# Kernel tuning notes

Hardware: AMD Instinct MI355X
Metric: run time of the kernel (lower is better)

Reference implementation:

```python
import math
import jax, jax.numpy as jnp
import numpy as np

B, S, HID = 1, 2048, 4096
NH, NKV, D = 32, 8, 128
THETA = 10000.0


def setup_inputs() -> dict:
    key = jax.random.key(0)
    k1, k2, k3, k4, k5 = jax.random.split(key, 5)
    hidden_states = jax.random.normal(k1, (B, S, HID), dtype=jnp.float32)
    k_cache = jax.random.normal(k2, (B, NKV, S, D), dtype=jnp.float32)
    v_cache = jax.random.normal(k3, (B, NKV, S, D), dtype=jnp.float32)
    Wq = jax.random.normal(k4, (HID, NH * D), dtype=jnp.float32) * 0.02
    Wo = jax.random.normal(k5, (NH * D, HID), dtype=jnp.float32) * 0.02
    position_ids = jnp.broadcast_to(jnp.arange(S, dtype=jnp.int32), (B, S))
    # causal mask: True = masked out (torch.where(mask, -10000, scores))
    attention_mask = jnp.broadcast_to(
        jnp.triu(jnp.ones((S, S), dtype=bool), k=1)[None, None], (B, 1, S, S)
    )
    return {
        "hidden_states": hidden_states,
        "k_cache": k_cache,
        "v_cache": v_cache,
        "Wq": Wq,
        "Wo": Wo,
        "position_ids": position_ids,
        "attention_mask": attention_mask,
    }


def _rotate_half(x):
    x1, x2 = jnp.split(x, 2, axis=-1)
    return jnp.concatenate([-x2, x1], axis=-1)


def _rope_tables(position_ids):
    # Llama rotary embedding gathered at position_ids -> [B, 1, S, D]
    inv_freq = 1.0 / (THETA ** (jnp.arange(0, D, 2, dtype=jnp.float32) / D))
    freqs = position_ids[..., None].astype(jnp.float32) * inv_freq  # [B, S, D/2]
    emb = jnp.concatenate([freqs, freqs], axis=-1)  # [B, S, D]
    return jnp.cos(emb)[:, None], jnp.sin(emb)[:, None]


def reference(hidden_states, k_cache, v_cache, Wq, Wo, position_ids, attention_mask):
    G = NH // NKV  # GQA group size
    # q projection: [B, S, HID] -> [B, NH, S, D]
    q = (hidden_states @ Wq).reshape(B, S, NH, D).transpose(0, 2, 1, 3)
    cos, sin = _rope_tables(position_ids)
    q = q * cos + _rotate_half(q) * sin
    # GQA without materializing repeat_kv: group query heads over kv heads
    qg = q.reshape(B, NKV, G, S, D)
    scores = jnp.einsum("bkgsd,bktd->bkgst", qg, k_cache) / math.sqrt(D)
    scores = scores.reshape(B, NH, S, S)
    scores = jnp.where(attention_mask, jnp.float32(-10000.0), scores)
    probs = jax.nn.softmax(scores.astype(jnp.float32), axis=-1).astype(q.dtype)
    out = jnp.einsum("bkgst,bktd->bkgsd", probs.reshape(B, NKV, G, S, S), v_cache)
    out = out.reshape(B, NH, S, D).transpose(0, 2, 1, 3).reshape(B, S, NH * D)
    return out @ Wo
```

## Files before the change

### kernel.cpp

```cpp
#include <hip/hip_runtime.h>
#include <cstdint>
#include <cstddef>

#define S_LEN 2048
#define HID 4096
#define NH 32
#define NKV 8
#define HD 128

typedef __attribute__((ext_vector_type(4))) float f32x4;
typedef __attribute__((ext_vector_type(8))) short bf16x8;

__device__ __forceinline__ unsigned short f2bf(float f) {
  union { float f; uint32_t u; } v; v.f = f;
  uint32_t r = v.u + 0x7FFFu + ((v.u >> 16) & 1u);
  return (unsigned short)(r >> 16);
}

__device__ __forceinline__ float exp2_fast(float x) {
#if __has_builtin(__builtin_amdgcn_exp2f)
  return __builtin_amdgcn_exp2f(x);
#else
  float r; asm("v_exp_f32 %0, %1" : "=v"(r) : "v"(x)); return r;
#endif
}

__device__ __forceinline__ unsigned int cvt_pk_bf16(float lo, float hi) {
  unsigned int r;
  asm("v_cvt_pk_bf16_f32 %0, %1, %2" : "=v"(r) : "v"(lo), "v"(hi));
  return r;
}

__global__ void cvt_bf16_kernel(const float* __restrict__ in,
                                unsigned short* __restrict__ out, int n4) {
  int i = blockIdx.x * blockDim.x + threadIdx.x;
  if (i >= n4) return;
  float4 v = ((const float4*)in)[i];
  ushort4 o;
  o.x = f2bf(v.x); o.y = f2bf(v.y); o.z = f2bf(v.z); o.w = f2bf(v.w);
  ((ushort4*)out)[i] = o;
}

__global__ __launch_bounds__(256) void transpose_cvt2_kernel(
    const float* __restrict__ in0, unsigned short* __restrict__ out0,
    const float* __restrict__ in1, unsigned short* __restrict__ out1,
    int R, int C) {
  __shared__ float tile[64][65];
  const float* inb = (blockIdx.z == 0) ? in0 : in1;
  unsigned short* outb = (blockIdx.z == 0) ? out0 : out1;
  const int c0 = blockIdx.x * 64, r0 = blockIdx.y * 64;
  const int tid = threadIdx.x;
#pragma unroll
  for (int p = 0; p < 4; ++p) {
    const int ch = p * 256 + tid;
    const int r = ch >> 4, off = (ch & 15) << 2;
    *(float4*)&tile[r][off] = *(const float4*)(inb + (size_t)(r0 + r) * C + c0 + off);
  }
  __syncthreads();
#pragma unroll
  for (int p = 0; p < 2; ++p) {
    const int ch = p * 256 + tid;
    const int i = ch >> 3, j0 = (ch & 7) << 3;
    bf16x8 v;
#pragma unroll
    for (int k = 0; k < 8; ++k) v[k] = (short)f2bf(tile[j0 + k][i]);
    *(bf16x8*)(outb + (size_t)(c0 + i) * R + r0 + j0) = v;
  }
}

__global__ __launch_bounds__(256) void transpose_cvt_kernel(
    const float* __restrict__ in, unsigned short* __restrict__ out, int R, int C) {
  __shared__ float tile[64][65];
  const int b = blockIdx.z;
  const float* inb = in + (size_t)b * R * C;
  unsigned short* outb = out + (size_t)b * R * C;
  const int c0 = blockIdx.x * 64, r0 = blockIdx.y * 64;
  const int tid = threadIdx.x;
#pragma unroll
  for (int p = 0; p < 4; ++p) {
    const int ch = p * 256 + tid;
    const int r = ch >> 4, off = (ch & 15) << 2;
    *(float4*)&tile[r][off] = *(const float4*)(inb + (size_t)(r0 + r) * C + c0 + off);
  }
  __syncthreads();
#pragma unroll
  for (int p = 0; p < 2; ++p) {
    const int ch = p * 256 + tid;
    const int i = ch >> 3, j0 = (ch & 7) << 3;
    bf16x8 v;
#pragma unroll
    for (int k = 0; k < 8; ++k) v[k] = (short)f2bf(tile[j0 + k][i]);
    *(bf16x8*)(outb + (size_t)(c0 + i) * R + r0 + j0) = v;
  }
}

__global__ __launch_bounds__(256, 2) void gemm_bt_kernel(
    const unsigned short* __restrict__ A, const unsigned short* __restrict__ BT,
    float* __restrict__ C, int M, int N, int K) {
  __shared__ __align__(16) unsigned short As[128 * 64];
  __shared__ __align__(16) unsigned short Bs[128 * 64];
  const int tid = threadIdx.x;
  const int lane = tid & 63;
  const int wid = tid >> 6;
  const int wm = (wid >> 1) * 64, wn = (wid & 1) * 64;
  const int g = blockIdx.x;
  const int xcd = g & 7, local = g >> 3;
  const int m0 = (xcd * 2 + (local & 1)) * 128;
  const int n0 = (local >> 1) * 128;
  const int lr = lane & 15;
  const int quad = lane >> 4;
  const int sw = lr & 7;
  f32x4 acc[4][4] = {};
  for (int kt = 0; kt < K; kt += 64) {
    __syncthreads();
#pragma unroll
    for (int p = 0; p < 4; ++p) {
      const int c = p * 256 + tid;
      const int r = c >> 3, jsrc = (c & 7) ^ (r & 7);
      __builtin_amdgcn_global_load_lds(
          (const __attribute__((address_space(1))) void*)(A + (size_t)(m0 + r) * K + kt + jsrc * 8),
          (__attribute__((address_space(3))) void*)(As + c * 8), 16, 0, 0);
      __builtin_amdgcn_global_load_lds(
          (const __attribute__((address_space(1))) void*)(BT + (size_t)(n0 + r) * K + kt + jsrc * 8),
          (__attribute__((address_space(3))) void*)(Bs + c * 8), 16, 0, 0);
    }
    __syncthreads();
#pragma unroll
    for (int h = 0; h < 2; ++h) {
      const int pos = ((h * 4 + quad) ^ sw) << 3;
      bf16x8 a[4], b[4];
#pragma unroll
      for (int t = 0; t < 4; ++t) {
        a[t] = *(const bf16x8*)(As + (wm + t * 16 + lr) * 64 + pos);
        b[t] = *(const bf16x8*)(Bs + (wn + t * 16 + lr) * 64 + pos);
      }
#pragma unroll
      for (int mt = 0; mt < 4; ++mt)
#pragma unroll
        for (int nt = 0; nt < 4; ++nt)
          acc[mt][nt] = __builtin_amdgcn_mfma_f32_16x16x32_bf16(a[mt], b[nt], acc[mt][nt], 0, 0, 0);
    }
  }
  const int qd = quad << 2;
#pragma unroll
  for (int mt = 0; mt < 4; ++mt)
#pragma unroll
    for (int nt = 0; nt < 4; ++nt) {
      const int row = m0 + wm + mt * 16 + qd;
      const int col = n0 + wn + nt * 16 + lr;
#pragma unroll
      for (int r = 0; r < 4; ++r)
        C[(size_t)(row + r) * N + col] = acc[mt][nt][r];
    }
}

__global__ __launch_bounds__(256, 2) void gemm_rope_kernel(
    const unsigned short* __restrict__ A, const unsigned short* __restrict__ BT,
    const int* __restrict__ pos_ids, unsigned short* __restrict__ Qout) {
  __shared__ __align__(16) unsigned short As[128 * 64];
  __shared__ __align__(16) unsigned short Bs[128 * 64];
  const int tid = threadIdx.x;
  const int lane = tid & 63;
  const int wid = tid >> 6;
  const int wm = wid * 32;
  const int g = blockIdx.x;
  const int xcd = g & 7, local = g >> 3;
  const int m0 = (xcd * 2 + (local & 1)) * 128;
  const int n0 = (local >> 1) * 128;
  const int lr = lane & 15;
  const int quad = lane >> 4;
  const int sw = lr & 7;
  f32x4 acc[2][8] = {};
  for (int kt = 0; kt < HID; kt += 64) {
    __syncthreads();
#pragma unroll
    for (int p = 0; p < 4; ++p) {
      const int c = p * 256 + tid;
      const int r = c >> 3, jsrc = (c & 7) ^ (r & 7);
      __builtin_amdgcn_global_load_lds(
          (const __attribute__((address_space(1))) void*)(A + (size_t)(m0 + r) * HID + kt + jsrc * 8),
          (__attribute__((address_space(3))) void*)(As + c * 8), 16, 0, 0);
      __builtin_amdgcn_global_load_lds(
          (const __attribute__((address_space(1))) void*)(BT + (size_t)(n0 + r) * HID + kt + jsrc * 8),
          (__attribute__((address_space(3))) void*)(Bs + c * 8), 16, 0, 0);
    }
    __syncthreads();
#pragma unroll
    for (int h = 0; h < 2; ++h) {
      const int pos = ((h * 4 + quad) ^ sw) << 3;
      bf16x8 a[2], b[8];
#pragma unroll
      for (int t = 0; t < 2; ++t)
        a[t] = *(const bf16x8*)(As + (wm + t * 16 + lr) * 64 + pos);
#pragma unroll
      for (int t = 0; t < 8; ++t)
        b[t] = *(const bf16x8*)(Bs + (t * 16 + lr) * 64 + pos);
#pragma unroll
      for (int mt = 0; mt < 2; ++mt)
#pragma unroll
        for (int nt = 0; nt < 8; ++nt)
          acc[mt][nt] = __builtin_amdgcn_mfma_f32_16x16x32_bf16(a[mt], b[nt], acc[mt][nt], 0, 0, 0);
    }
  }
  const int qd = quad << 2;
  const int h = n0 >> 7;
#pragma unroll
  for (int mt = 0; mt < 2; ++mt)
#pragma unroll
    for (int r = 0; r < 4; ++r) {
      const int row = m0 + wm + mt * 16 + qd + r;
      const float pos = (float)pos_ids[row];
#pragma unroll
      for (int nt = 0; nt < 4; ++nt) {
        const int i = nt * 16 + lr;
        const float invf = __expf(-(float)(2 * i) * (9.2103403719761836f / 128.0f));
        float sn, cs;
        __sincosf(pos * invf, &sn, &cs);
        const float x1 = acc[mt][nt][r], x2 = acc[mt][nt + 4][r];
        Qout[((size_t)h * S_LEN + row) * HD + i]      = f2bf(x1 * cs - x2 * sn);
        Qout[((size_t)h * S_LEN + row) * HD + i + 64] = f2bf(x2 * cs + x1 * sn);
      }
    }
}

__global__ __launch_bounds__(256, 2) void attn_kernel(
    const unsigned short* __restrict__ Q, const unsigned short* __restrict__ Kc,
    const unsigned short* __restrict__ VT, unsigned short* __restrict__ Aout) {
  __shared__ __align__(16) unsigned short Ks[2][64 * 128];
  __shared__ __align__(16) unsigned short Vs[2][128 * 64];
  const int tid = threadIdx.x, lane = tid & 63, wid = tid >> 6;
  const int qh = blockIdx.x;
  const int qt = (blockIdx.y < 8) ? (15 - (int)blockIdx.y) : ((int)blockIdx.y - 8);
  const int kvh = qh >> 2;
  const int lr = lane & 15, quad = lane >> 4;
  const float SC = 0.12751619754705767f;
  const float NB = -23.083120654223414f;

  bf16x8 qf[2][4];
#pragma unroll
  for (int mt = 0; mt < 2; ++mt)
#pragma unroll
    for (int kk = 0; kk < 4; ++kk)
      qf[mt][kk] = *(const bf16x8*)(Q + ((size_t)qh * S_LEN + qt * 128 + wid * 32 + mt * 16 + lr) * HD + kk * 32 + quad * 8);

  f32x4 o[2][8] = {};
  float lsum[2] = {0.f, 0.f};
  const int nkt = 2 * qt + 2;
  const int swz = lr & 7;

  auto stage = [&](int buf, int kt2) {
#pragma unroll
    for (int p = 0; p < 4; ++p) {
      const int c = p * 256 + tid;
      const int kr = c >> 4, kj = (c & 15) ^ (kr & 7);
      __builtin_amdgcn_global_load_lds(
          (const __attribute__((address_space(1))) void*)(Kc + ((size_t)kvh * S_LEN + kt2 * 64 + kr) * HD + kj * 8),
          (__attribute__((address_space(3))) void*)(&Ks[buf][c * 8]), 16, 0, 0);
      const int vr = c >> 3, vj = (c & 7) ^ (vr & 7);
      __builtin_amdgcn_global_load_lds(
          (const __attribute__((address_space(1))) void*)(VT + ((size_t)kvh * HD + vr) * S_LEN + kt2 * 64 + vj * 8),
          (__attribute__((address_space(3))) void*)(&Vs[buf][c * 8]), 16, 0, 0);
    }
  };

  stage(0, 0);
  __syncthreads();

  for (int kt2 = 0; kt2 < nkt; ++kt2) {
    const int cur = kt2 & 1;
    if (kt2 + 1 < nkt) stage(cur ^ 1, kt2 + 1);
    const unsigned short* KsC = Ks[cur];
    const unsigned short* VsC = Vs[cur];
    const bool dtile = (kt2 >= 2 * qt);

    uint32_t Pw[2][4][2];
#pragma unroll
    for (int nt = 0; nt < 4; ++nt) {
      f32x4 s0 = {}, s1 = {};
      __builtin_amdgcn_s_setprio(1);
#pragma unroll
      for (int kk = 0; kk < 4; ++kk) {
        bf16x8 kf = *(const bf16x8*)(KsC + (nt * 16 + lr) * 128 + (((kk * 4 + quad) ^ swz) * 8));
        s0 = __builtin_amdgcn_mfma_f32_16x16x32_bf16(kf, qf[0][kk], s0, 0, 0, 0);
        s1 = __builtin_amdgcn_mfma_f32_16x16x32_bf16(kf, qf[1][kk], s1, 0, 0, 0);
      }
      __builtin_amdgcn_s_setprio(0);
      const int skey0 = kt2 * 64 + nt * 16 + quad * 4;
#pragma unroll
      for (int mt = 0; mt < 2; ++mt) {
        const f32x4 s = mt ? s1 : s0;
        const int qrow = qt * 128 + wid * 32 + mt * 16 + lr;
        float pv[4];
        float ls = 0.f;
#pragma unroll
        for (int r = 0; r < 4; ++r) {
          float v = fmaf(s[r], SC, NB);
          if (dtile && (skey0 + r) > qrow) v = -1e30f;
          pv[r] = exp2_fast(v);
          ls += pv[r];
        }
        lsum[mt] += ls;
        Pw[mt][nt][0] = cvt_pk_bf16(pv[0], pv[1]);
        Pw[mt][nt][1] = cvt_pk_bf16(pv[2], pv[3]);
      }
    }

    bf16x8 pf[2][2];
#pragma unroll
    for (int mt = 0; mt < 2; ++mt)
#pragma unroll
      for (int k = 0; k < 2; ++k) {
        uint32_t w4[4];
#pragma unroll
        for (int w = 0; w < 2; ++w) {
          uint32_t x = Pw[mt][2 * k][w], y = Pw[mt][2 * k + 1][w];
          asm("v_permlane32_swap_b32 %0, %1" : "+v"(x), "+v"(y));
          uint32_t xe = x, xo = x;
          asm("v_permlane16_swap_b32 %0, %1" : "+v"(xe), "+v"(xo));
          uint32_t ye = y, yo = y;
          asm("v_permlane16_swap_b32 %0, %1" : "+v"(ye), "+v"(yo));
          const bool qodd = (quad & 1) != 0;
          w4[0 + w] = qodd ? ye : xe;
          w4[2 + w] = qodd ? yo : xo;
        }
        union { uint32_t u[4]; bf16x8 v; } P;
        P.u[0] = w4[0]; P.u[1] = w4[1]; P.u[2] = w4[2]; P.u[3] = w4[3];
        pf[mt][k] = P.v;
      }

    __builtin_amdgcn_s_setprio(1);
#pragma unroll
    for (int dt = 0; dt < 8; ++dt)
#pragma unroll
      for (int kk = 0; kk < 2; ++kk) {
        bf16x8 vf = *(const bf16x8*)(VsC + (dt * 16 + lr) * 64 + (((kk * 4 + quad) ^ swz) * 8));
        o[0][dt] = __builtin_amdgcn_mfma_f32_16x16x32_bf16(vf, pf[0][kk], o[0][dt], 0, 0, 0);
        o[1][dt] = __builtin_amdgcn_mfma_f32_16x16x32_bf16(vf, pf[1][kk], o[1][dt], 0, 0, 0);
      }
    __builtin_amdgcn_s_setprio(0);

    __syncthreads();
  }

#pragma unroll
  for (int mt = 0; mt < 2; ++mt) {
    float l = lsum[mt];
    l += __shfl_xor(l, 16);
    l += __shfl_xor(l, 32);
    const float inv = 1.0f / l;
    const int qrow = qt * 128 + wid * 32 + mt * 16 + lr;
#pragma unroll
    for (int dt = 0; dt < 8; ++dt) {
      uint2 w;
      w.x = cvt_pk_bf16(o[mt][dt][0] * inv, o[mt][dt][1] * inv);
      w.y = cvt_pk_bf16(o[mt][dt][2] * inv, o[mt][dt][3] * inv);
      *(uint2*)(Aout + (size_t)qrow * HID + qh * HD + dt * 16 + quad * 4) = w;
    }
  }
}

extern "C" void kernel_launch(void* const* d_in, const int* in_sizes, int n_in,
                              void* d_out, int out_size, void* d_ws, size_t ws_size,
                              hipStream_t stream) {
  const float* hidden  = (const float*)d_in[0];
  const float* k_cache = (const float*)d_in[1];
  const float* v_cache = (const float*)d_in[2];
  const float* Wq      = (const float*)d_in[3];
  const float* Wo      = (const float*)d_in[4];
  const int*   pos     = (const int*)d_in[5];
  float* out = (float*)d_out;

  char* ws = (char*)d_ws;
  unsigned short* hidden_bf = (unsigned short*)(ws + 0);
  unsigned short* attn_bf   = hidden_bf;
  unsigned short* WqT       = (unsigned short*)(ws + 16777216);
  unsigned short* WoT       = (unsigned short*)(ws + 50331648);
  unsigned short* k_bf      = (unsigned short*)(ws + 83886080);
  unsigned short* vT        = (unsigned short*)(ws + 88080384);
  unsigned short* q_bf      = (unsigned short*)(ws + 92274688);

  cvt_bf16_kernel<<<(S_LEN * HID / 4 + 255) / 256, 256, 0, stream>>>(hidden, hidden_bf, S_LEN * HID / 4);
  cvt_bf16_kernel<<<(NKV * S_LEN * HD / 4 + 255) / 256, 256, 0, stream>>>(k_cache, k_bf, NKV * S_LEN * HD / 4);
  transpose_cvt2_kernel<<<dim3(HID / 64, HID / 64, 2), 256, 0, stream>>>(Wq, WqT, Wo, WoT, HID, HID);
  transpose_cvt_kernel<<<dim3(HD / 64, S_LEN / 64, NKV), 256, 0, stream>>>(v_cache, vT, S_LEN, HD);

  gemm_rope_kernel<<<dim3((S_LEN / 128) * (HID / 128)), 256, 0, stream>>>(hidden_bf, WqT, pos, q_bf);
  attn_kernel<<<dim3(NH, S_LEN / 128), 256, 0, stream>>>(q_bf, k_bf, vT, attn_bf);
  gemm_bt_kernel<<<dim3((S_LEN / 128) * (HID / 128)), 256, 0, stream>>>(attn_bf, WoT, out, S_LEN, HID, HID);
}
```

Baseline: 427.6 us.

## Triple-buffer GEMM LDS staging with 128x256 tiles and 512-thread blocks

Both projection GEMMs (Q-with-RoPE and output) now use 512-thread blocks on 128x256 output tiles and a three-stage LDS ring. Global-to-LDS loads for tile t+2 are issued while tile t is computed, with a partial vmcnt wait and a single barrier per K step in place of the two syncthreads around synchronous loading. MFMA sections are wrapped in raised wave priority. The intent is to hide global-load latency and halve the B-tile reloads per output element, at the cost of much more LDS per block (144 KB), which may limit occupancy to one block per CU. The grid also drops to 256 blocks.

```diff
diff --git a/kernel.cpp b/kernel.cpp
--- a/kernel.cpp
+++ b/kernel.cpp
@@ -94,52 +94,74 @@
   }
 }
 
-__global__ __launch_bounds__(256, 2) void gemm_bt_kernel(
+__global__ __launch_bounds__(512, 2) void gemm_bt_kernel(
     const unsigned short* __restrict__ A, const unsigned short* __restrict__ BT,
     float* __restrict__ C, int M, int N, int K) {
-  __shared__ __align__(16) unsigned short As[128 * 64];
-  __shared__ __align__(16) unsigned short Bs[128 * 64];
+  __shared__ __align__(16) unsigned short As[3][128 * 64];
+  __shared__ __align__(16) unsigned short Bs[3][256 * 64];
   const int tid = threadIdx.x;
   const int lane = tid & 63;
   const int wid = tid >> 6;
-  const int wm = (wid >> 1) * 64, wn = (wid & 1) * 64;
+  const int wm = (wid >> 2) * 64;
+  const int wn = (wid & 3) * 64;
   const int g = blockIdx.x;
-  const int xcd = g & 7, local = g >> 3;
-  const int m0 = (xcd * 2 + (local & 1)) * 128;
-  const int n0 = (local >> 1) * 128;
+  const int wg = (g & 7) * 32 + (g >> 3);
+  const int m0 = (wg & 15) * 128;
+  const int n0 = (wg >> 4) * 256;
   const int lr = lane & 15;
   const int quad = lane >> 4;
   const int sw = lr & 7;
+  const int nkt = K >> 6;
+
+  auto stage = [&](int buf, int kt) {
+#pragma unroll
+    for (int p = 0; p < 2; ++p) {
+      const int c = p * 512 + tid;
+      const int r = c >> 3, j = (c & 7) ^ (r & 7);
+      __builtin_amdgcn_global_load_lds(
+          (const __attribute__((address_space(1))) void*)(A + (size_t)(m0 + r) * K + kt * 64 + j * 8),
+          (__attribute__((address_space(3))) void*)(&As[buf][c * 8]), 16, 0, 0);
+    }
+#pragma unroll
+    for (int p = 0; p < 4; ++p) {
+      const int c = p * 512 + tid;
+      const int r = c >> 3, j = (c & 7) ^ (r & 7);
+      __builtin_amdgcn_global_load_lds(
+          (const __attribute__((address_space(1))) void*)(BT + (size_t)(n0 + r) * K + kt * 64 + j * 8),
+          (__attribute__((address_space(3))) void*)(&Bs[buf][c * 8]), 16, 0, 0);
+    }
+  };
+
   f32x4 acc[4][4] = {};
-  for (int kt = 0; kt < K; kt += 64) {
-    __syncthreads();
-#pragma unroll
-    for (int p = 0; p < 4; ++p) {
-      const int c = p * 256 + tid;
-      const int r = c >> 3, jsrc = (c & 7) ^ (r & 7);
-      __builtin_amdgcn_global_load_lds(
-          (const __attribute__((address_space(1))) void*)(A + (size_t)(m0 + r) * K + kt + jsrc * 8),
-          (__attribute__((address_space(3))) void*)(As + c * 8), 16, 0, 0);
-      __builtin_amdgcn_global_load_lds(
-          (const __attribute__((address_space(1))) void*)(BT + (size_t)(n0 + r) * K + kt + jsrc * 8),
-          (__attribute__((address_space(3))) void*)(Bs + c * 8), 16, 0, 0);
-    }
-    __syncthreads();
+  stage(0, 0);
+  stage(1, 1);
+  int buf = 0;
+  for (int t = 0; t < nkt; ++t) {
+    if (t + 1 < nkt) asm volatile("s_waitcnt vmcnt(6)" ::: "memory");
+    else             asm volatile("s_waitcnt vmcnt(0)" ::: "memory");
+    __builtin_amdgcn_s_barrier();
+    asm volatile("" ::: "memory");
+    if (t + 2 < nkt) { int nb = buf + 2; if (nb >= 3) nb -= 3; stage(nb, t + 2); }
+    const unsigned short* as = As[buf];
+    const unsigned short* bs = Bs[buf];
 #pragma unroll
     for (int h = 0; h < 2; ++h) {
       const int pos = ((h * 4 + quad) ^ sw) << 3;
       bf16x8 a[4], b[4];
 #pragma unroll
-      for (int t = 0; t < 4; ++t) {
-        a[t] = *(const bf16x8*)(As + (wm + t * 16 + lr) * 64 + pos);
-        b[t] = *(const bf16x8*)(Bs + (wn + t * 16 + lr) * 64 + pos);
-      }
+      for (int tq = 0; tq < 4; ++tq) {
+        a[tq] = *(const bf16x8*)(as + (wm + tq * 16 + lr) * 64 + pos);
+        b[tq] = *(const bf16x8*)(bs + (wn + tq * 16 + lr) * 64 + pos);
+      }
+      __builtin_amdgcn_s_setprio(1);
 #pragma unroll
       for (int mt = 0; mt < 4; ++mt)
 #pragma unroll
         for (int nt = 0; nt < 4; ++nt)
           acc[mt][nt] = __builtin_amdgcn_mfma_f32_16x16x32_bf16(a[mt], b[nt], acc[mt][nt], 0, 0, 0);
-    }
+      __builtin_amdgcn_s_setprio(0);
+    }
+    ++buf; if (buf >= 3) buf -= 3;
   }
   const int qd = quad << 2;
 #pragma unroll
@@ -154,56 +176,78 @@
     }
 }
 
-__global__ __launch_bounds__(256, 2) void gemm_rope_kernel(
+__global__ __launch_bounds__(512, 2) void gemm_rope_kernel(
     const unsigned short* __restrict__ A, const unsigned short* __restrict__ BT,
     const int* __restrict__ pos_ids, unsigned short* __restrict__ Qout) {
-  __shared__ __align__(16) unsigned short As[128 * 64];
-  __shared__ __align__(16) unsigned short Bs[128 * 64];
+  __shared__ __align__(16) unsigned short As[3][128 * 64];
+  __shared__ __align__(16) unsigned short Bs[3][256 * 64];
   const int tid = threadIdx.x;
   const int lane = tid & 63;
   const int wid = tid >> 6;
-  const int wm = wid * 32;
+  const int wm = (wid >> 1) * 32;
+  const int wn = (wid & 1) * 128;
   const int g = blockIdx.x;
-  const int xcd = g & 7, local = g >> 3;
-  const int m0 = (xcd * 2 + (local & 1)) * 128;
-  const int n0 = (local >> 1) * 128;
+  const int wg = (g & 7) * 32 + (g >> 3);
+  const int m0 = (wg & 15) * 128;
+  const int n0 = (wg >> 4) * 256;
   const int lr = lane & 15;
   const int quad = lane >> 4;
   const int sw = lr & 7;
+  const int nkt = HID >> 6;
+
+  auto stage = [&](int buf, int kt) {
+#pragma unroll
+    for (int p = 0; p < 2; ++p) {
+      const int c = p * 512 + tid;
+      const int r = c >> 3, j = (c & 7) ^ (r & 7);
+      __builtin_amdgcn_global_load_lds(
+          (const __attribute__((address_space(1))) void*)(A + (size_t)(m0 + r) * HID + kt * 64 + j * 8),
+          (__attribute__((address_space(3))) void*)(&As[buf][c * 8]), 16, 0, 0);
+    }
+#pragma unroll
+    for (int p = 0; p < 4; ++p) {
+      const int c = p * 512 + tid;
+      const int r = c >> 3, j = (c & 7) ^ (r & 7);
+      __builtin_amdgcn_global_load_lds(
+          (const __attribute__((address_space(1))) void*)(BT + (size_t)(n0 + r) * HID + kt * 64 + j * 8),
+          (__attribute__((address_space(3))) void*)(&Bs[buf][c * 8]), 16, 0, 0);
+    }
+  };
+
   f32x4 acc[2][8] = {};
-  for (int kt = 0; kt < HID; kt += 64) {
-    __syncthreads();
-#pragma unroll
-    for (int p = 0; p < 4; ++p) {
-      const int c = p * 256 + tid;
-      const int r = c >> 3, jsrc = (c & 7) ^ (r & 7);
-      __builtin_amdgcn_global_load_lds(
-          (const __attribute__((address_space(1))) void*)(A + (size_t)(m0 + r) * HID + kt + jsrc * 8),
-          (__attribute__((address_space(3))) void*)(As + c * 8), 16, 0, 0);
-      __builtin_amdgcn_global_load_lds(
-          (const __attribute__((address_space(1))) void*)(BT + (size_t)(n0 + r) * HID + kt + jsrc * 8),
-          (__attribute__((address_space(3))) void*)(Bs + c * 8), 16, 0, 0);
-    }
-    __syncthreads();
+  stage(0, 0);
+  stage(1, 1);
+  int buf = 0;
+  for (int t = 0; t < nkt; ++t) {
+    if (t + 1 < nkt) asm volatile("s_waitcnt vmcnt(6)" ::: "memory");
+    else             asm volatile("s_waitcnt vmcnt(0)" ::: "memory");
+    __builtin_amdgcn_s_barrier();
+    asm volatile("" ::: "memory");
+    if (t + 2 < nkt) { int nb = buf + 2; if (nb >= 3) nb -= 3; stage(nb, t + 2); }
+    const unsigned short* as = As[buf];
+    const unsigned short* bs = Bs[buf];
 #pragma unroll
     for (int h = 0; h < 2; ++h) {
       const int pos = ((h * 4 + quad) ^ sw) << 3;
       bf16x8 a[2], b[8];
 #pragma unroll
-      for (int t = 0; t < 2; ++t)
-        a[t] = *(const bf16x8*)(As + (wm + t * 16 + lr) * 64 + pos);
-#pragma unroll
-      for (int t = 0; t < 8; ++t)
-        b[t] = *(const bf16x8*)(Bs + (t * 16 + lr) * 64 + pos);
+      for (int tq = 0; tq < 2; ++tq)
+        a[tq] = *(const bf16x8*)(as + (wm + tq * 16 + lr) * 64 + pos);
+#pragma unroll
+      for (int tq = 0; tq < 8; ++tq)
+        b[tq] = *(const bf16x8*)(bs + (wn + tq * 16 + lr) * 64 + pos);
+      __builtin_amdgcn_s_setprio(1);
 #pragma unroll
       for (int mt = 0; mt < 2; ++mt)
 #pragma unroll
         for (int nt = 0; nt < 8; ++nt)
           acc[mt][nt] = __builtin_amdgcn_mfma_f32_16x16x32_bf16(a[mt], b[nt], acc[mt][nt], 0, 0, 0);
-    }
+      __builtin_amdgcn_s_setprio(0);
+    }
+    ++buf; if (buf >= 3) buf -= 3;
   }
   const int qd = quad << 2;
-  const int h = n0 >> 7;
+  const int h = (n0 + wn) >> 7;
 #pragma unroll
   for (int mt = 0; mt < 2; ++mt)
 #pragma unroll
@@ -384,7 +428,7 @@
   transpose_cvt2_kernel<<<dim3(HID / 64, HID / 64, 2), 256, 0, stream>>>(Wq, WqT, Wo, WoT, HID, HID);
   transpose_cvt_kernel<<<dim3(HD / 64, S_LEN / 64, NKV), 256, 0, stream>>>(v_cache, vT, S_LEN, HD);
 
-  gemm_rope_kernel<<<dim3((S_LEN / 128) * (HID / 128)), 256, 0, stream>>>(hidden_bf, WqT, pos, q_bf);
+  gemm_rope_kernel<<<dim3((S_LEN / 128) * (HID / 256)), 512, 0, stream>>>(hidden_bf, WqT, pos, q_bf);
   attn_kernel<<<dim3(NH, S_LEN / 128), 256, 0, stream>>>(q_bf, k_bf, vT, attn_bf);
-  gemm_bt_kernel<<<dim3((S_LEN / 128) * (HID / 128)), 256, 0, stream>>>(attn_bf, WoT, out, S_LEN, HID, HID);
-}
+  gemm_bt_kernel<<<dim3((S_LEN / 128) * (HID / 256)), 512, 0, stream>>>(attn_bf, WoT, out, S_LEN, HID, HID);
+}
```

Result: slower. 464.8 us (+8.7%).
